# Kernel tuning notes

Hardware: AMD Instinct MI355X
Metric: run time of the kernel (lower is better)

## Reference

```python
import jax, jax.numpy as jnp
import numpy as np

B, T, F, U, NIDS = 1024, 64, 18, 128, 1000


def setup_inputs() -> dict:
    key = jax.random.key(0)
    ks = jax.random.split(key, 8)
    feats = jax.random.normal(ks[0], (B, T, F), dtype=jnp.float32)
    # column 0 holds card ids as floats (cast to int32 inside the cell)
    ids = jax.random.randint(ks[1], (B, T), 0, NIDS).astype(jnp.float32)
    inputs = feats.at[:, :, 0].set(ids)
    sync_states = jnp.zeros((NIDS, B, U), dtype=jnp.float32)
    kernel = jax.random.normal(ks[2], (F, 3 * U), dtype=jnp.float32) * 0.1
    rec_kernel = jax.random.normal(ks[3], (U, 3 * U), dtype=jnp.float32) * 0.1
    bias = jnp.zeros((3 * U,), dtype=jnp.float32)
    dense_w = jax.random.normal(ks[4], (U, 64), dtype=jnp.float32) * 0.1
    dense_b = jnp.zeros((64,), dtype=jnp.float32)
    out_w = jax.random.normal(ks[5], (64, 1), dtype=jnp.float32) * 0.1
    out_b = jnp.zeros((1,), dtype=jnp.float32)
    return dict(inputs=inputs, sync_states=sync_states, kernel=kernel,
                rec_kernel=rec_kernel, bias=bias, dense_w=dense_w,
                dense_b=dense_b, out_w=out_w, out_b=out_b)


def _hard_sigmoid(x):
    # keras hard_sigmoid
    return jnp.clip(0.2 * x + 0.5, 0.0, 1.0)


def reference(inputs, sync_states, kernel, rec_kernel, bias, dense_w, dense_b, out_w, out_b):
    batch_idx = jnp.arange(B)

    def step(table, x_t):  # x_t: [B, F]
        ids = x_t[:, 0].astype(jnp.int32)            # card ids
        h = table[ids, batch_idx]                    # gather_nd: [B, U]
        xz = x_t @ kernel + bias                     # [B, 3U]
        hz = h @ rec_kernel                          # [B, 3U]
        z = _hard_sigmoid(xz[:, :U] + hz[:, :U])
        r = _hard_sigmoid(xz[:, U:2 * U] + hz[:, U:2 * U])
        hh = jnp.tanh(xz[:, 2 * U:] + r * hz[:, 2 * U:])
        h_new = z * h + (1.0 - z) * hh               # [B, U]
        table = table.at[ids, batch_idx].set(h_new)  # scatter_nd_update
        return table, h_new

    _, hs = jax.lax.scan(step, sync_states, jnp.transpose(inputs, (1, 0, 2)))
    last = hs[-1]                                    # RNN returns last output
    d = jax.nn.relu(last @ dense_w + dense_b)        # dropout inactive at inference
    out = jax.nn.sigmoid(d @ out_w + out_b)          # [B, 1]
    return out
```

## Files before the change

kernel.cpp:

```cpp
#include <hip/hip_runtime.h>
#include <math.h>

#define B_   1024
#define T_   64
#define F_   18
#define U_   128
#define U3_  384
#define D_   64

__global__ __launch_bounds__(128) void feedzai_sync_gru_kernel(
    const float* __restrict__ inputs,
    const float* __restrict__ sync_states,
    const float* __restrict__ kernel_,
    const float* __restrict__ rec_kernel,
    const float* __restrict__ bias,
    const float* __restrict__ dense_w,
    const float* __restrict__ dense_b,
    const float* __restrict__ out_w,
    const float* __restrict__ out_b,
    float* __restrict__ out)
{
    const int b = blockIdx.x;
    const int u = threadIdx.x;

    __shared__ float sh[U_];
    __shared__ float sx[F_];
    __shared__ int   sid[T_];
    __shared__ int   s_flag;

    const float* inp_b = inputs + (size_t)b * T_ * F_;

    if (u < T_) sid[u] = (int)inp_b[u * F_ + 0];
    __syncthreads();

    const int id_last = sid[T_ - 1];

    float hu = sync_states[((size_t)id_last * B_ + b) * U_ + u];
    sh[u] = hu;
    __syncthreads();

    for (int t = 0; t < T_; ++t) {
        if (sid[t] != id_last) continue;

        if (u < F_) sx[u] = inp_b[t * F_ + u];
        if (u == 0) s_flag = 0;
        __syncthreads();

        hu = sh[u];
        if (hu != 0.0f) s_flag = 1;

        float xz_z = bias[u];
        float xz_r = bias[U_ + u];
        float xz_h = bias[2 * U_ + u];
        #pragma unroll
        for (int f = 0; f < F_; ++f) {
            const float xv = sx[f];
            const float* kf = kernel_ + f * U3_;
            xz_z += xv * kf[u];
            xz_r += xv * kf[U_ + u];
            xz_h += xv * kf[2 * U_ + u];
        }
        __syncthreads();

        float hz_z = 0.0f, hz_r = 0.0f, hz_h = 0.0f;
        if (s_flag) {
            for (int k = 0; k < U_; ++k) {
                const float hv = sh[k];
                const float* rk = rec_kernel + k * U3_;
                hz_z += hv * rk[u];
                hz_r += hv * rk[U_ + u];
                hz_h += hv * rk[2 * U_ + u];
            }
        }

        const float z  = fminf(fmaxf(0.2f * (xz_z + hz_z) + 0.5f, 0.0f), 1.0f);
        const float r  = fminf(fmaxf(0.2f * (xz_r + hz_r) + 0.5f, 0.0f), 1.0f);
        const float hh = tanhf(xz_h + r * hz_h);
        const float hn = z * hu + (1.0f - z) * hh;

        __syncthreads();
        sh[u] = hn;
        __syncthreads();
    }

    float dv = 0.0f;
    if (u < D_) {
        dv = dense_b[u];
        for (int k = 0; k < U_; ++k)
            dv += sh[k] * dense_w[k * D_ + u];
        dv = fmaxf(dv, 0.0f);
        dv *= out_w[u];

        #pragma unroll
        for (int off = 32; off > 0; off >>= 1)
            dv += __shfl_down(dv, off, 64);

        if (u == 0)
            out[b] = 1.0f / (1.0f + expf(-(dv + out_b[0])));
    }
}

extern "C" void kernel_launch(void* const* d_in, const int* in_sizes, int n_in,
                              void* d_out, int out_size, void* d_ws, size_t ws_size,
                              hipStream_t stream) {
    const float* inputs      = (const float*)d_in[0];
    const float* sync_states = (const float*)d_in[1];
    const float* kernel_     = (const float*)d_in[2];
    const float* rec_kernel  = (const float*)d_in[3];
    const float* bias        = (const float*)d_in[4];
    const float* dense_w     = (const float*)d_in[5];
    const float* dense_b     = (const float*)d_in[6];
    const float* out_w       = (const float*)d_in[7];
    const float* out_b       = (const float*)d_in[8];
    float* out = (float*)d_out;

    feedzai_sync_gru_kernel<<<dim3(B_), dim3(128), 0, stream>>>(
        inputs, sync_states, kernel_, rec_kernel, bias,
        dense_w, dense_b, out_w, out_b, out);
}
```

Measured before the change: 581.1 us.

## Run each batch row on a single wavefront using shuffles instead of shared memory

```diff
diff --git a/kernel.cpp b/kernel.cpp
--- a/kernel.cpp
+++ b/kernel.cpp
@@ -8,7 +8,7 @@
 #define U3_  384
 #define D_   64
 
-__global__ __launch_bounds__(128) void feedzai_sync_gru_kernel(
+__global__ __launch_bounds__(64) void feedzai_sync_gru_kernel(
     const float* __restrict__ inputs,
     const float* __restrict__ sync_states,
     const float* __restrict__ kernel_,
@@ -23,81 +23,82 @@
     const int b = blockIdx.x;
     const int u = threadIdx.x;
 
-    __shared__ float sh[U_];
-    __shared__ float sx[F_];
-    __shared__ int   sid[T_];
-    __shared__ int   s_flag;
-
     const float* inp_b = inputs + (size_t)b * T_ * F_;
 
-    if (u < T_) sid[u] = (int)inp_b[u * F_ + 0];
-    __syncthreads();
+    const int id_t = (int)inp_b[u * F_ + 0];
+    const int id_last = __shfl(id_t, T_ - 1, 64);
+    unsigned long long mask = __ballot(id_t == id_last);
 
-    const int id_last = sid[T_ - 1];
+    const float* hptr = sync_states + ((size_t)id_last * B_ + b) * U_;
+    float h0 = hptr[u];
+    float h1 = hptr[u + 64];
 
-    float hu = sync_states[((size_t)id_last * B_ + b) * U_ + u];
-    sh[u] = hu;
-    __syncthreads();
+    while (mask) {
+        const int t = __builtin_ctzll(mask);
+        mask &= mask - 1;
 
-    for (int t = 0; t < T_; ++t) {
-        if (sid[t] != id_last) continue;
+        const float xv_own = (u < F_) ? inp_b[t * F_ + u] : 0.0f;
 
-        if (u < F_) sx[u] = inp_b[t * F_ + u];
-        if (u == 0) s_flag = 0;
-        __syncthreads();
-
-        hu = sh[u];
-        if (hu != 0.0f) s_flag = 1;
-
-        float xz_z = bias[u];
-        float xz_r = bias[U_ + u];
-        float xz_h = bias[2 * U_ + u];
+        float az0 = bias[u],           az1 = bias[u + 64];
+        float ar0 = bias[U_ + u],      ar1 = bias[U_ + u + 64];
+        float ah0 = bias[2 * U_ + u],  ah1 = bias[2 * U_ + u + 64];
         #pragma unroll
         for (int f = 0; f < F_; ++f) {
-            const float xv = sx[f];
+            const float xv = __shfl(xv_own, f, 64);
             const float* kf = kernel_ + f * U3_;
-            xz_z += xv * kf[u];
-            xz_r += xv * kf[U_ + u];
-            xz_h += xv * kf[2 * U_ + u];
+            az0 += xv * kf[u];            az1 += xv * kf[u + 64];
+            ar0 += xv * kf[U_ + u];       ar1 += xv * kf[U_ + u + 64];
+            ah0 += xv * kf[2 * U_ + u];   ah1 += xv * kf[2 * U_ + u + 64];
         }
-        __syncthreads();
 
-        float hz_z = 0.0f, hz_r = 0.0f, hz_h = 0.0f;
-        if (s_flag) {
-            for (int k = 0; k < U_; ++k) {
-                const float hv = sh[k];
+        float hz_z0 = 0.0f, hz_z1 = 0.0f;
+        float hz_r0 = 0.0f, hz_r1 = 0.0f;
+        float hz_h0 = 0.0f, hz_h1 = 0.0f;
+        if (__ballot((h0 != 0.0f) || (h1 != 0.0f)) != 0ULL) {
+            for (int k = 0; k < 64; ++k) {
+                const float hv = __shfl(h0, k, 64);
                 const float* rk = rec_kernel + k * U3_;
-                hz_z += hv * rk[u];
-                hz_r += hv * rk[U_ + u];
-                hz_h += hv * rk[2 * U_ + u];
+                hz_z0 += hv * rk[u];            hz_z1 += hv * rk[u + 64];
+                hz_r0 += hv * rk[U_ + u];       hz_r1 += hv * rk[U_ + u + 64];
+                hz_h0 += hv * rk[2 * U_ + u];   hz_h1 += hv * rk[2 * U_ + u + 64];
+            }
+            for (int k = 0; k < 64; ++k) {
+                const float hv = __shfl(h1, k, 64);
+                const float* rk = rec_kernel + (k + 64) * U3_;
+                hz_z0 += hv * rk[u];            hz_z1 += hv * rk[u + 64];
+                hz_r0 += hv * rk[U_ + u];       hz_r1 += hv * rk[U_ + u + 64];
+                hz_h0 += hv * rk[2 * U_ + u];   hz_h1 += hv * rk[2 * U_ + u + 64];
             }
         }
 
-        const float z  = fminf(fmaxf(0.2f * (xz_z + hz_z) + 0.5f, 0.0f), 1.0f);
-        const float r  = fminf(fmaxf(0.2f * (xz_r + hz_r) + 0.5f, 0.0f), 1.0f);
-        const float hh = tanhf(xz_h + r * hz_h);
-        const float hn = z * hu + (1.0f - z) * hh;
-
-        __syncthreads();
-        sh[u] = hn;
-        __syncthreads();
+        const float z0 = fminf(fmaxf(0.2f * (az0 + hz_z0) + 0.5f, 0.0f), 1.0f);
+        const float z1 = fminf(fmaxf(0.2f * (az1 + hz_z1) + 0.5f, 0.0f), 1.0f);
+        const float r0 = fminf(fmaxf(0.2f * (ar0 + hz_r0) + 0.5f, 0.0f), 1.0f);
+        const float r1 = fminf(fmaxf(0.2f * (ar1 + hz_r1) + 0.5f, 0.0f), 1.0f);
+        const float hh0 = tanhf(ah0 + r0 * hz_h0);
+        const float hh1 = tanhf(ah1 + r1 * hz_h1);
+        h0 = z0 * h0 + (1.0f - z0) * hh0;
+        h1 = z1 * h1 + (1.0f - z1) * hh1;
     }
 
-    float dv = 0.0f;
-    if (u < D_) {
-        dv = dense_b[u];
-        for (int k = 0; k < U_; ++k)
-            dv += sh[k] * dense_w[k * D_ + u];
-        dv = fmaxf(dv, 0.0f);
-        dv *= out_w[u];
+    float dv = dense_b[u];
+    for (int k = 0; k < 64; ++k) {
+        const float hv = __shfl(h0, k, 64);
+        dv += hv * dense_w[k * D_ + u];
+    }
+    for (int k = 0; k < 64; ++k) {
+        const float hv = __shfl(h1, k, 64);
+        dv += hv * dense_w[(k + 64) * D_ + u];
+    }
+    dv = fmaxf(dv, 0.0f);
+    dv *= out_w[u];
 
-        #pragma unroll
-        for (int off = 32; off > 0; off >>= 1)
-            dv += __shfl_down(dv, off, 64);
+    #pragma unroll
+    for (int off = 32; off > 0; off >>= 1)
+        dv += __shfl_down(dv, off, 64);
 
-        if (u == 0)
-            out[b] = 1.0f / (1.0f + expf(-(dv + out_b[0])));
-    }
+    if (u == 0)
+        out[b] = 1.0f / (1.0f + expf(-(dv + out_b[0])));
 }
 
 extern "C" void kernel_launch(void* const* d_in, const int* in_sizes, int n_in,
@@ -114,7 +115,7 @@
     const float* out_b       = (const float*)d_in[8];
     float* out = (float*)d_out;
 
-    feedzai_sync_gru_kernel<<<dim3(B_), dim3(128), 0, stream>>>(
+    feedzai_sync_gru_kernel<<<dim3(B_), dim3(64), 0, stream>>>(
         inputs, sync_states, kernel_, rec_kernel, bias,
         dense_w, dense_b, out_w, out_b, out);
 }
```

Measured after the change: 591.0 us. Within noise of the previous version (+1.7%).
